# Kernel tuning notes

Hardware: AMD Instinct MI355X
Metric: run time of the kernel (lower is better)

## Reference

```python
import jax, jax.numpy as jnp
import numpy as np

CHANNELS = [64, 128, 256, 512, 512]
RES = [256, 128, 64, 32, 16]
N = 8          # batch
NQ = 128       # n_quad
NCW = 128      # nc_w (output descriptor size)
GRAD_BOOST = 10.0


def _norm(x):
    # Norm module: per-sample, per-row normalization over last dim; torch std is unbiased (ddof=1)
    m = jnp.mean(x, axis=-1, keepdims=True)
    s = jnp.std(x, axis=-1, ddof=1, keepdims=True)
    return (x - m) / (s + 1e-8)


def _quad(x, w):
    # Quad_module: (M^T @ softmax(grad_boost*w, axis=0))**2, summed over spatial dim
    n, c, h, wd = x.shape
    M = x.reshape(n, c, h * wd)                      # (N, C, HW)
    sm = jax.nn.softmax(w * GRAD_BOOST, axis=0)      # (C, NQ)
    proj = jnp.einsum('nch,co->nho', M, sm)          # (N, HW, NQ)
    return jnp.sum(proj ** 2, axis=1)                # (N, NQ)


def setup_inputs() -> dict:
    key = jax.random.key(0)
    ks = jax.random.split(key, 20)
    inp = {}
    for i, (c, r) in enumerate(zip(CHANNELS, RES)):
        inp[f"x{i}"] = jax.random.normal(ks[i], (N, c, r, r), dtype=jnp.float32)
        # torch init: 5/grad_boost * rand(n_in, n_out) = 0.5 * U[0,1)
        inp[f"w1_{i}"] = 0.5 * jax.random.uniform(ks[5 + i], (c, NQ), dtype=jnp.float32)
    d_in = len(CHANNELS) * NQ
    inp["fc1_w"] = jax.random.normal(ks[10], (d_in, 512), dtype=jnp.float32) * 0.04
    inp["fc1_b"] = jnp.zeros((512,), dtype=jnp.float32)
    inp["fc2_w"] = jax.random.normal(ks[11], (512, 512), dtype=jnp.float32) * 0.04
    inp["fc2_b"] = jnp.zeros((512,), dtype=jnp.float32)
    inp["fc3_w"] = jax.random.normal(ks[12], (512, NCW), dtype=jnp.float32) * 0.04
    inp["fc3_b"] = jnp.zeros((NCW,), dtype=jnp.float32)
    return inp


def reference(x0, x1, x2, x3, x4, w1_0, w1_1, w1_2, w1_3, w1_4,
              fc1_w, fc1_b, fc2_w, fc2_b, fc3_w, fc3_b):
    xs = [x0, x1, x2, x3, x4]
    ws = [w1_0, w1_1, w1_2, w1_3, w1_4]
    feats = [_norm(_quad(x, w)) for x, w in zip(xs, ws)]  # each (N, NQ)
    h = jnp.concatenate(feats, axis=1)                    # (N, 5*NQ)
    h = jax.nn.leaky_relu(_norm(h @ fc1_w + fc1_b), 0.01)
    h = jax.nn.leaky_relu(_norm(h @ fc2_w + fc2_b), 0.01)
    return h @ fc3_w + fc3_b                              # (N, NCW)
```

## Files before the change

### kernel.cpp

```cpp
#include <hip/hip_runtime.h>
#include <hip/hip_bf16.h>
#include <stdint.h>

#define NQ 128
#define NLVL 5

typedef float  floatx4 __attribute__((ext_vector_type(4)));
typedef short  short8  __attribute__((ext_vector_type(8)));

__device__ __forceinline__ uint16_t f2bf(float f) {
    uint32_t u = __builtin_bit_cast(uint32_t, f);
    uint32_t r = u + 0x7FFFu + ((u >> 16) & 1u);
    return (uint16_t)(r >> 16);
}
__device__ __forceinline__ uint32_t pack2(float a, float b) {
    return (uint32_t)f2bf(a) | ((uint32_t)f2bf(b) << 16);
}
__device__ __forceinline__ float bf2f(uint16_t u) {
    return __builtin_bit_cast(float, (uint32_t)u << 16);
}
__device__ __forceinline__ short8 cvt8(float4 lo, float4 hi) {
    union { short8 s; uint32_t u[4]; } r;
    r.u[0] = pack2(lo.x, lo.y);
    r.u[1] = pack2(lo.z, lo.w);
    r.u[2] = pack2(hi.x, hi.y);
    r.u[3] = pack2(hi.z, hi.w);
    return r.s;
}
__device__ __forceinline__ void split_hilo(float4 v0, float4 v1, short8& hi, short8& lo) {
    hi = cvt8(v0, v1);
    float4 r0, r1;
    r0.x = v0.x - bf2f((uint16_t)hi[0]); r0.y = v0.y - bf2f((uint16_t)hi[1]);
    r0.z = v0.z - bf2f((uint16_t)hi[2]); r0.w = v0.w - bf2f((uint16_t)hi[3]);
    r1.x = v1.x - bf2f((uint16_t)hi[4]); r1.y = v1.y - bf2f((uint16_t)hi[5]);
    r1.z = v1.z - bf2f((uint16_t)hi[6]); r1.w = v1.w - bf2f((uint16_t)hi[7]);
    lo = cvt8(r0, r1);
}

#define MFMA16(a, b, c) __builtin_amdgcn_mfma_f32_16x16x32_bf16((a), (b), (c), 0, 0, 0)


struct AParams {
    const float* x0; const float* x1;
    float*       g0; float*       g1;
    const float* w[NLVL];
    uint16_t*    smT[NLVL];
    int          C[NLVL];
};

__device__ __forceinline__ void gram_tile_diag(
    const float* __restrict__ base, int ldr, int k0, int nst,
    int m, int kg, floatx4 (&acc)[4][4])
{
    float4 Alo[4], Ahi[4], Blo[4], Bhi[4];
    {
        int k = k0 + kg * 8;
        #pragma unroll
        for (int f = 0; f < 4; ++f) {
            const float* q = base + (size_t)(f * 16 + m) * ldr + k;
            Alo[f] = *(const float4*)q; Ahi[f] = *(const float4*)(q + 4);
        }
    }
    for (int s = 0; s < nst; s += 2) {
        if (s + 1 < nst) {
            int k1 = k0 + (s + 1) * 32 + kg * 8;
            #pragma unroll
            for (int f = 0; f < 4; ++f) {
                const float* q = base + (size_t)(f * 16 + m) * ldr + k1;
                Blo[f] = *(const float4*)q; Bhi[f] = *(const float4*)(q + 4);
            }
        }
        {
            short8 fr[4];
            #pragma unroll
            for (int f = 0; f < 4; ++f) fr[f] = cvt8(Alo[f], Ahi[f]);
            #pragma unroll
            for (int rf = 0; rf < 4; ++rf)
                #pragma unroll
                for (int cf = 0; cf < 4; ++cf)
                    acc[rf][cf] = MFMA16(fr[rf], fr[cf], acc[rf][cf]);
        }
        if (s + 2 < nst) {
            int k2 = k0 + (s + 2) * 32 + kg * 8;
            #pragma unroll
            for (int f = 0; f < 4; ++f) {
                const float* q = base + (size_t)(f * 16 + m) * ldr + k2;
                Alo[f] = *(const float4*)q; Ahi[f] = *(const float4*)(q + 4);
            }
        }
        if (s + 1 < nst) {
            short8 fr[4];
            #pragma unroll
            for (int f = 0; f < 4; ++f) fr[f] = cvt8(Blo[f], Bhi[f]);
            #pragma unroll
            for (int rf = 0; rf < 4; ++rf)
                #pragma unroll
                for (int cf = 0; cf < 4; ++cf)
                    acc[rf][cf] = MFMA16(fr[rf], fr[cf], acc[rf][cf]);
        }
    }
}

__device__ __forceinline__ void gram_tile_off(
    const float* __restrict__ ab, const float* __restrict__ bb,
    int ldr, int k0, int nst, int m, int kg, floatx4 (&acc)[4][4])
{
    #pragma unroll 2
    for (int s = 0; s < nst; ++s) {
        int k = k0 + s * 32 + kg * 8;
        float4 a0[4], a1[4], b0[4], b1[4];
        #pragma unroll
        for (int f = 0; f < 4; ++f) {
            const float* qa = ab + (size_t)(f * 16 + m) * ldr + k;
            const float* qb = bb + (size_t)(f * 16 + m) * ldr + k;
            a0[f] = *(const float4*)qa; a1[f] = *(const float4*)(qa + 4);
            b0[f] = *(const float4*)qb; b1[f] = *(const float4*)(qb + 4);
        }
        short8 af[4], bf[4];
        #pragma unroll
        for (int f = 0; f < 4; ++f) {
            af[f] = cvt8(a0[f], a1[f]);
            bf[f] = cvt8(b0[f], b1[f]);
        }
        #pragma unroll
        for (int rf = 0; rf < 4; ++rf)
            #pragma unroll
            for (int cf = 0; cf < 4; ++cf)
                acc[rf][cf] = MFMA16(af[rf], bf[cf], acc[rf][cf]);
    }
}

__global__ __launch_bounds__(256) void gram_sm_kernel(AParams p) {
    __shared__ float gred[4096];
    int b  = blockIdx.x;
    int t  = threadIdx.x;
    int wv = t >> 6, lane = t & 63, m = lane & 15, kg = lane >> 4;

    if (b >= 320) {
        int idx = (b - 320) * 4 + wv;
        int lvl = idx >> 7, o = idx & 127;
        int C   = p.C[lvl];
        const float* w = p.w[lvl];
        float ev[8];
        int nIter = C >> 6;
        float mx = -1e30f;
        for (int it = 0; it < nIter; ++it) {
            float z = 10.0f * w[(size_t)(it * 64 + lane) * NQ + o];
            ev[it] = z;
            mx = fmaxf(mx, z);
        }
        #pragma unroll
        for (int s = 32; s; s >>= 1) mx = fmaxf(mx, __shfl_xor(mx, s));
        float sum = 0.f;
        for (int it = 0; it < nIter; ++it) { ev[it] = expf(ev[it] - mx); sum += ev[it]; }
        #pragma unroll
        for (int s = 32; s; s >>= 1) sum += __shfl_xor(sum, s);
        float inv = 1.0f / sum;
        uint16_t* dst = p.smT[lvl] + (size_t)o * C;
        for (int it = 0; it < nIter; ++it) dst[it * 64 + lane] = f2bf(ev[it] * inv);
        return;
    }

    floatx4 acc[4][4];
    floatx4 zero = {0.f, 0.f, 0.f, 0.f};
    #pragma unroll
    for (int i = 0; i < 4; ++i)
        #pragma unroll
        for (int j = 0; j < 4; ++j) acc[i][j] = zero;

    if (b < 256) {
        int n = b >> 5, ch = b & 31;
        const float* xb = p.x0 + (size_t)n * 64 * 65536;
        int k0 = ch * 2048 + wv * 512;
        gram_tile_diag(xb, 65536, k0, 16, m, kg, acc);

        for (int i = t; i < 4096; i += 256) gred[i] = 0.f;
        __syncthreads();
        #pragma unroll
        for (int rf = 0; rf < 4; ++rf)
            #pragma unroll
            for (int cf = 0; cf < 4; ++cf)
                #pragma unroll
                for (int r = 0; r < 4; ++r)
                    atomicAdd(&gred[(rf * 16 + kg * 4 + r) * 64 + cf * 16 + m],
                              acc[rf][cf][r]);
        __syncthreads();
        float* gb = p.g0 + (size_t)n * 4096;
        for (int i = t; i < 4096; i += 256) atomicAdd(&gb[i], gred[i]);
    } else {
        int b2 = b - 256;
        int n = b2 >> 3, kc = b2 & 7;
        const float* xb = p.x1 + (size_t)n * 128 * 16384;
        int rb = wv >> 1, cb = wv & 1;
        const float* ab = xb + (size_t)rb * 64 * 16384;
        const float* bb = xb + (size_t)cb * 64 * 16384;
        int k0 = kc * 2048;
        if (rb == cb) gram_tile_diag(ab, 16384, k0, 64, m, kg, acc);
        else          gram_tile_off(ab, bb, 16384, k0, 64, m, kg, acc);
        float* gb = p.g1 + (size_t)n * 16384;
        #pragma unroll
        for (int rf = 0; rf < 4; ++rf)
            #pragma unroll
            for (int cf = 0; cf < 4; ++cf)
                #pragma unroll
                for (int r = 0; r < 4; ++r)
                    atomicAdd(&gb[(size_t)(rb * 64 + rf * 16 + kg * 4 + r) * 128 +
                                  cb * 64 + cf * 16 + m],
                              acc[rf][cf][r]);
    }
}


struct QSParams {
    const float*    x[3];
    const uint16_t* smT[3];
    float*          quad;
    int             C[3];
    int             HW[3];
    int             blk_base[3];
    int             quad_blocks;
    const float*    g0; const float* g1;
    const uint16_t* smT0; const uint16_t* smT1;
};

template<int C>
__device__ __forceinline__ void sgs_direct(const float* __restrict__ g,
                                           const uint16_t* __restrict__ smT,
                                           float* __restrict__ qdst) {
    constexpr int RF  = C / 64;
    constexpr int KSL = C / 32;
    int t = threadIdx.x;
    int wv = t >> 6, lane = t & 63, m = lane & 15, kg = lane >> 4;
    floatx4 acc[RF][8];
    floatx4 zero = {0.f, 0.f, 0.f, 0.f};
    #pragma unroll
    for (int rf = 0; rf < RF; ++rf)
        #pragma unroll
        for (int ot = 0; ot < 8; ++ot) acc[rf][ot] = zero;

    #pragma unroll
    for (int ksl = 0; ksl < KSL; ++ksl) {
        short8 bfr[8];
        #pragma unroll
        for (int ot = 0; ot < 8; ++ot)
            bfr[ot] = *(const short8*)(smT + (size_t)(ot * 16 + m) * C + ksl * 32 + kg * 8);
        #pragma unroll
        for (int rf = 0; rf < RF; ++rf) {
            const float* gp = g + (size_t)((wv * RF + rf) * 16 + m) * C + ksl * 32 + kg * 8;
            float4 v0 = *(const float4*)gp, v1 = *(const float4*)(gp + 4);
            short8 ah, al;
            split_hilo(v0, v1, ah, al);
            #pragma unroll
            for (int ot = 0; ot < 8; ++ot) {
                acc[rf][ot] = MFMA16(ah, bfr[ot], acc[rf][ot]);
                acc[rf][ot] = MFMA16(al, bfr[ot], acc[rf][ot]);
            }
        }
    }
    #pragma unroll
    for (int ot = 0; ot < 8; ++ot) {
        float part = 0.f;
        #pragma unroll
        for (int rf = 0; rf < RF; ++rf) {
            int c0 = (wv * RF + rf) * 16 + kg * 4;
            #pragma unroll
            for (int r = 0; r < 4; ++r) {
                float sv = bf2f(smT[(size_t)(ot * 16 + m) * C + c0 + r]);
                part = fmaf(sv, acc[rf][ot][r], part);
            }
        }
        part += __shfl_xor(part, 16);
        part += __shfl_xor(part, 32);
        if (lane < 16) atomicAdd(qdst + (size_t)(ot * 16 + lane) * 16, part);
    }
}

__global__ __launch_bounds__(256) void quad_sgs_kernel(QSParams p) {
    __shared__ __align__(16) short At[64 * 40];
    __shared__ __align__(16) short Bt[128 * 40];

    int bid = blockIdx.x;
    if (bid >= p.quad_blocks) {
        int b = bid - p.quad_blocks;
        int lvl = b >> 3, n = b & 7;
        if (lvl == 0)
            sgs_direct<64>(p.g0 + (size_t)n * 4096, p.smT0,
                           p.quad + (size_t)n * 2048);
        else
            sgs_direct<128>(p.g1 + (size_t)n * 16384, p.smT1,
                            p.quad + (size_t)(8 + n) * 2048);
        return;
    }

    int lvl = 0;
    #pragma unroll
    for (int l = 1; l < 3; ++l) if (bid >= p.blk_base[l]) lvl = l;
    int rel = bid - p.blk_base[lvl];
    int n   = rel & 7;
    int ht  = rel >> 3;
    int C   = p.C[lvl];
    int HW  = p.HW[lvl];
    int h0  = ht * 64;

    const float*    xb  = p.x[lvl] + (size_t)n * C * HW + h0;
    const uint16_t* smT = p.smT[lvl];

    int t    = threadIdx.x;
    int wave = t >> 6;
    int lane = t & 63;
    int m    = lane & 15;
    int kg   = lane >> 4;

    floatx4 acc[4][2];
    floatx4 zero = {0.f, 0.f, 0.f, 0.f};
    #pragma unroll
    for (int i = 0; i < 4; ++i)
        #pragma unroll
        for (int j = 0; j < 2; ++j) acc[i][j] = zero;

    int c_l = (t & 15) * 2;
    int h_l = (t >> 4) * 4;

    for (int c0 = 0; c0 < C; c0 += 32) {
        const float* s1 = xb + (size_t)(c0 + c_l) * HW + h_l;
        float4 a4 = *(const float4*)s1;
        float4 b4 = *(const float4*)(s1 + HW);
        #pragma unroll
        for (int j = 0; j < 4; ++j) {
            uint32_t pk = (uint32_t)f2bf(((const float*)&a4)[j]) |
                          ((uint32_t)f2bf(((const float*)&b4)[j]) << 16);
            *(uint32_t*)&At[(h_l + j) * 40 + c_l] = pk;
        }
        #pragma unroll
        for (int it = 0; it < 2; ++it) {
            int idx  = it * 256 + t;
            int o    = idx >> 2;
            int part = idx & 3;
            uint4 v = *(const uint4*)(smT + (size_t)o * C + c0 + part * 8);
            *(uint4*)&Bt[o * 40 + part * 8] = v;
        }
        __syncthreads();

        short8 af[4];
        #pragma unroll
        for (int mt = 0; mt < 4; ++mt)
            af[mt] = *(const short8*)&At[(mt * 16 + m) * 40 + kg * 8];
        short8 bfr[2];
        #pragma unroll
        for (int ot = 0; ot < 2; ++ot)
            bfr[ot] = *(const short8*)&Bt[((wave * 2 + ot) * 16 + m) * 40 + kg * 8];
        #pragma unroll
        for (int mt = 0; mt < 4; ++mt)
            #pragma unroll
            for (int ot = 0; ot < 2; ++ot)
                acc[mt][ot] = MFMA16(af[mt], bfr[ot], acc[mt][ot]);
        __syncthreads();
    }

    float* qbase = p.quad + (size_t)((lvl + 2) * 8 + n) * 128 * 16;
    #pragma unroll
    for (int ot = 0; ot < 2; ++ot) {
        float part = 0.f;
        #pragma unroll
        for (int mt = 0; mt < 4; ++mt)
            #pragma unroll
            for (int r = 0; r < 4; ++r) {
                float v = acc[mt][ot][r];
                part = fmaf(v, v, part);
            }
        part += __shfl_xor(part, 16);
        part += __shfl_xor(part, 32);
        if (lane < 16) {
            int o = (wave * 2 + ot) * 16 + lane;
            atomicAdd(qbase + (size_t)o * 16, part);
        }
    }
}

__global__ __launch_bounds__(256) void hfc1_kernel(
    const float* __restrict__ quad, const float* __restrict__ w,
    const float* __restrict__ b, float* __restrict__ h1) {
    __shared__ float feat[640];
    __shared__ float stats[10];
    __shared__ float part[256];
    int blk = blockIdx.x;
    int n = blk >> 3, c8 = blk & 7;
    int t = threadIdx.x;
    for (int idx = t; idx < 640; idx += 256) {
        int L = idx >> 7, o = idx & 127;
        feat[idx] = quad[((size_t)(L * 8 + n) * 128 + o) * 16];
    }
    __syncthreads();
    int wv = t >> 6, lane = t & 63;
    for (int L = wv; L < 5; L += 4) {
        float a = feat[L * 128 + lane], c = feat[L * 128 + 64 + lane];
        float s = a + c;
        #pragma unroll
        for (int sh = 32; sh; sh >>= 1) s += __shfl_xor(s, sh);
        float mean = s * (1.f / 128.f);
        float d0 = a - mean, d1 = c - mean;
        float v = d0 * d0 + d1 * d1;
        #pragma unroll
        for (int sh = 32; sh; sh >>= 1) v += __shfl_xor(v, sh);
        if (lane == 0) {
            stats[L]     = mean;
            stats[5 + L] = 1.f / (sqrtf(v * (1.f / 127.f)) + 1e-8f);
        }
    }
    __syncthreads();
    for (int idx = t; idx < 640; idx += 256) {
        int L = idx >> 7;
        feat[idx] = (feat[idx] - stats[L]) * stats[5 + L];
    }
    __syncthreads();

    float acc = 0.f;
    const float* wc = w + c8 * 64 + lane;
    int k0 = wv * 160;
    #pragma unroll 8
    for (int k = k0; k < k0 + 160; ++k) acc = fmaf(feat[k], wc[(size_t)k * 512], acc);
    part[t] = acc;
    __syncthreads();
    if (t < 64) {
        float r = part[t] + part[t + 64] + part[t + 128] + part[t + 192];
        h1[(size_t)n * 512 + c8 * 64 + t] = r + b[c8 * 64 + t];
    }
}

__device__ __forceinline__ void norm_leaky_512(float* buf, float* red, int t) {
    float a = buf[t], c = buf[t + 256];
    float s = a + c;
    #pragma unroll
    for (int sh = 32; sh; sh >>= 1) s += __shfl_xor(s, sh);
    if ((t & 63) == 0) red[t >> 6] = s;
    __syncthreads();
    float mean = (red[0] + red[1] + red[2] + red[3]) * (1.f / 512.f);
    float d0 = a - mean, d1 = c - mean;
    float v = d0 * d0 + d1 * d1;
    #pragma unroll
    for (int sh = 32; sh; sh >>= 1) v += __shfl_xor(v, sh);
    __syncthreads();
    if ((t & 63) == 0) red[t >> 6] = v;
    __syncthreads();
    float inv = 1.f / (sqrtf((red[0] + red[1] + red[2] + red[3]) * (1.f / 511.f)) + 1e-8f);
    float n0 = d0 * inv, n1 = d1 * inv;
    buf[t]       = n0 > 0.f ? n0 : 0.01f * n0;
    buf[t + 256] = n1 > 0.f ? n1 : 0.01f * n1;
    __syncthreads();
}

__global__ __launch_bounds__(256) void hfc2_kernel(
    const float* __restrict__ h1, const float* __restrict__ w,
    const float* __restrict__ b, float* __restrict__ h2) {
    __shared__ float buf[512];
    __shared__ float red[4];
    __shared__ float part[256];
    int blk = blockIdx.x;
    int n = blk >> 3, c8 = blk & 7;
    int t = threadIdx.x;
    buf[t]       = h1[(size_t)n * 512 + t];
    buf[t + 256] = h1[(size_t)n * 512 + t + 256];
    __syncthreads();
    norm_leaky_512(buf, red, t);
    int wv = t >> 6, lane = t & 63;
    float acc = 0.f;
    const float* wc = w + c8 * 64 + lane;
    int k0 = wv * 128;
    #pragma unroll 8
    for (int k = k0; k < k0 + 128; ++k) acc = fmaf(buf[k], wc[(size_t)k * 512], acc);
    part[t] = acc;
    __syncthreads();
    if (t < 64) {
        float r = part[t] + part[t + 64] + part[t + 128] + part[t + 192];
        h2[(size_t)n * 512 + c8 * 64 + t] = r + b[c8 * 64 + t];
    }
}

__global__ __launch_bounds__(256) void hfc3_kernel(
    const float* __restrict__ h2, const float* __restrict__ w,
    const float* __restrict__ b, float* __restrict__ out) {
    __shared__ float buf[512];
    __shared__ float red[4];
    __shared__ float part[256];
    int blk = blockIdx.x;
    int n = blk >> 1, c2 = blk & 1;
    int t = threadIdx.x;
    buf[t]       = h2[(size_t)n * 512 + t];
    buf[t + 256] = h2[(size_t)n * 512 + t + 256];
    __syncthreads();
    norm_leaky_512(buf, red, t);
    int wv = t >> 6, lane = t & 63;
    float acc = 0.f;
    const float* wc = w + c2 * 64 + lane;
    int k0 = wv * 128;
    #pragma unroll 8
    for (int k = k0; k < k0 + 128; ++k) acc = fmaf(buf[k], wc[(size_t)k * 128], acc);
    part[t] = acc;
    __syncthreads();
    if (t < 64) {
        out[(size_t)n * 128 + c2 * 64 + t] =
            part[t] + part[t + 64] + part[t + 128] + part[t + 192] + b[c2 * 64 + t];
    }
}

extern "C" void kernel_launch(void* const* d_in, const int* in_sizes, int n_in,
                              void* d_out, int out_size, void* d_ws, size_t ws_size,
                              hipStream_t stream) {
    static const int Cs[NLVL]   = {64, 128, 256, 512, 512};
    static const int RESs[NLVL] = {256, 128, 64, 32, 16};

    const float* x[NLVL];
    const float* w[NLVL];
    for (int i = 0; i < NLVL; ++i) {
        x[i] = (const float*)d_in[2 * i];
        w[i] = (const float*)d_in[2 * i + 1];
    }
    const float* fc1_w = (const float*)d_in[10];
    const float* fc1_b = (const float*)d_in[11];
    const float* fc2_w = (const float*)d_in[12];
    const float* fc2_b = (const float*)d_in[13];
    const float* fc3_w = (const float*)d_in[14];
    const float* fc3_b = (const float*)d_in[15];

    uint16_t* smT_base = (uint16_t*)d_ws;
    int smOff[NLVL];
    int off = 0;
    for (int i = 0; i < NLVL; ++i) { smOff[i] = off; off += Cs[i] * NQ; }
    size_t smBytes = (size_t)off * sizeof(uint16_t);
    float* quad = (float*)((char*)d_ws + smBytes);
    size_t quadFloats = (size_t)NLVL * 8 * NQ * 16;
    float* g0 = quad + quadFloats;
    float* g1 = g0 + (size_t)8 * 64 * 64;
    float* h1 = g1 + (size_t)8 * 128 * 128;
    float* h2 = h1 + (size_t)8 * 512;
    size_t zeroBytes = (quadFloats + (size_t)8 * 64 * 64 + (size_t)8 * 128 * 128) * sizeof(float);

    hipMemsetAsync(quad, 0, zeroBytes, stream);

    AParams ap;
    ap.x0 = x[0]; ap.x1 = x[1]; ap.g0 = g0; ap.g1 = g1;
    for (int i = 0; i < NLVL; ++i) {
        ap.w[i]   = w[i];
        ap.smT[i] = smT_base + smOff[i];
        ap.C[i]   = Cs[i];
    }
    gram_sm_kernel<<<480, 256, 0, stream>>>(ap);

    QSParams qp;
    int base = 0;
    for (int i = 0; i < 3; ++i) {
        int lvl = i + 2;
        qp.x[i]   = x[lvl];
        qp.smT[i] = smT_base + smOff[lvl];
        qp.C[i]   = Cs[lvl];
        qp.HW[i]  = RESs[lvl] * RESs[lvl];
        qp.blk_base[i] = base;
        base += (RESs[lvl] * RESs[lvl] / 64) * 8;
    }
    qp.quad = quad;
    qp.quad_blocks = base;
    qp.g0 = g0; qp.g1 = g1;
    qp.smT0 = smT_base + smOff[0];
    qp.smT1 = smT_base + smOff[1];
    quad_sgs_kernel<<<base + 16, 256, 0, stream>>>(qp);

    hfc1_kernel<<<64, 256, 0, stream>>>(quad, fc1_w, fc1_b, h1);
    hfc2_kernel<<<64, 256, 0, stream>>>(h1, fc2_w, fc2_b, h2);
    hfc3_kernel<<<16, 256, 0, stream>>>(h2, fc3_w, fc3_b, (float*)d_out);
}
```

Before: 483.6 us.

## Stage Gram-matrix tiles through LDS as bf16 and widen blocks to 512 threads

The Gram kernels for levels 0 and 1 now load fp32 input chunks cooperatively, convert them to bf16 once, and stage them in padded shared memory. Waves then read MFMA fragments from there, where before each wave loaded and converted its own fragments directly from global memory. Blocks grow to 512 threads with more blocks per level, so each wave computes a smaller slice of the output tile. This removes redundant global loads and conversions, especially for level 1's off-diagonal tiles, at the cost of extra barriers per step and more atomic reductions into the global Gram buffer.

After: 423.9 us. -12.3%, faster.

```diff
diff --git a/kernel.cpp b/kernel.cpp
--- a/kernel.cpp
+++ b/kernel.cpp
@@ -48,96 +48,14 @@
     int          C[NLVL];
 };
 
-__device__ __forceinline__ void gram_tile_diag(
-    const float* __restrict__ base, int ldr, int k0, int nst,
-    int m, int kg, floatx4 (&acc)[4][4])
-{
-    float4 Alo[4], Ahi[4], Blo[4], Bhi[4];
-    {
-        int k = k0 + kg * 8;
-        #pragma unroll
-        for (int f = 0; f < 4; ++f) {
-            const float* q = base + (size_t)(f * 16 + m) * ldr + k;
-            Alo[f] = *(const float4*)q; Ahi[f] = *(const float4*)(q + 4);
-        }
-    }
-    for (int s = 0; s < nst; s += 2) {
-        if (s + 1 < nst) {
-            int k1 = k0 + (s + 1) * 32 + kg * 8;
-            #pragma unroll
-            for (int f = 0; f < 4; ++f) {
-                const float* q = base + (size_t)(f * 16 + m) * ldr + k1;
-                Blo[f] = *(const float4*)q; Bhi[f] = *(const float4*)(q + 4);
-            }
-        }
-        {
-            short8 fr[4];
-            #pragma unroll
-            for (int f = 0; f < 4; ++f) fr[f] = cvt8(Alo[f], Ahi[f]);
-            #pragma unroll
-            for (int rf = 0; rf < 4; ++rf)
-                #pragma unroll
-                for (int cf = 0; cf < 4; ++cf)
-                    acc[rf][cf] = MFMA16(fr[rf], fr[cf], acc[rf][cf]);
-        }
-        if (s + 2 < nst) {
-            int k2 = k0 + (s + 2) * 32 + kg * 8;
-            #pragma unroll
-            for (int f = 0; f < 4; ++f) {
-                const float* q = base + (size_t)(f * 16 + m) * ldr + k2;
-                Alo[f] = *(const float4*)q; Ahi[f] = *(const float4*)(q + 4);
-            }
-        }
-        if (s + 1 < nst) {
-            short8 fr[4];
-            #pragma unroll
-            for (int f = 0; f < 4; ++f) fr[f] = cvt8(Blo[f], Bhi[f]);
-            #pragma unroll
-            for (int rf = 0; rf < 4; ++rf)
-                #pragma unroll
-                for (int cf = 0; cf < 4; ++cf)
-                    acc[rf][cf] = MFMA16(fr[rf], fr[cf], acc[rf][cf]);
-        }
-    }
-}
-
-__device__ __forceinline__ void gram_tile_off(
-    const float* __restrict__ ab, const float* __restrict__ bb,
-    int ldr, int k0, int nst, int m, int kg, floatx4 (&acc)[4][4])
-{
-    #pragma unroll 2
-    for (int s = 0; s < nst; ++s) {
-        int k = k0 + s * 32 + kg * 8;
-        float4 a0[4], a1[4], b0[4], b1[4];
-        #pragma unroll
-        for (int f = 0; f < 4; ++f) {
-            const float* qa = ab + (size_t)(f * 16 + m) * ldr + k;
-            const float* qb = bb + (size_t)(f * 16 + m) * ldr + k;
-            a0[f] = *(const float4*)qa; a1[f] = *(const float4*)(qa + 4);
-            b0[f] = *(const float4*)qb; b1[f] = *(const float4*)(qb + 4);
-        }
-        short8 af[4], bf[4];
-        #pragma unroll
-        for (int f = 0; f < 4; ++f) {
-            af[f] = cvt8(a0[f], a1[f]);
-            bf[f] = cvt8(b0[f], b1[f]);
-        }
-        #pragma unroll
-        for (int rf = 0; rf < 4; ++rf)
-            #pragma unroll
-            for (int cf = 0; cf < 4; ++cf)
-                acc[rf][cf] = MFMA16(af[rf], bf[cf], acc[rf][cf]);
-    }
-}
-
-__global__ __launch_bounds__(256) void gram_sm_kernel(AParams p) {
-    __shared__ float gred[4096];
-    int b  = blockIdx.x;
-    int t  = threadIdx.x;
+__global__ __launch_bounds__(512, 5) void gram_sm_kernel(AParams p) {
+    __shared__ __align__(16) short lds[2 * 64 * 72];
+    int b = blockIdx.x;
+    int t = threadIdx.x;
     int wv = t >> 6, lane = t & 63, m = lane & 15, kg = lane >> 4;
 
-    if (b >= 320) {
-        int idx = (b - 320) * 4 + wv;
+    if (b >= 768) {
+        int idx = (b - 768) * 8 + wv;
         int lvl = idx >> 7, o = idx & 127;
         int C   = p.C[lvl];
         const float* w = p.w[lvl];
@@ -161,51 +79,128 @@
         return;
     }
 
-    floatx4 acc[4][4];
-    floatx4 zero = {0.f, 0.f, 0.f, 0.f};
-    #pragma unroll
-    for (int i = 0; i < 4; ++i)
-        #pragma unroll
-        for (int j = 0; j < 4; ++j) acc[i][j] = zero;
-
-    if (b < 256) {
-        int n = b >> 5, ch = b & 31;
+    if (b < 512) {
+        int n = b >> 6, ch = b & 63;
         const float* xb = p.x0 + (size_t)n * 64 * 65536;
-        int k0 = ch * 2048 + wv * 512;
-        gram_tile_diag(xb, 65536, k0, 16, m, kg, acc);
-
-        for (int i = t; i < 4096; i += 256) gred[i] = 0.f;
+        int rg = wv & 3, kh = wv >> 2;
+        short* buf = lds + kh * (64 * 72);
+        int tg = t & 255;
+        int k0 = ch * 1024 + kh * 512;
+
+        floatx4 acc[4];
+        floatx4 zero = {0.f, 0.f, 0.f, 0.f};
+        #pragma unroll
+        for (int cf = 0; cf < 4; ++cf) acc[cf] = zero;
+
+        float4 v[4];
+        #pragma unroll
+        for (int j = 0; j < 4; ++j) {
+            int fid = j * 256 + tg;
+            v[j] = *(const float4*)(xb + (size_t)(fid >> 4) * 65536 + k0 + (fid & 15) * 4);
+        }
+        for (int s = 0; s < 8; ++s) {
+            __syncthreads();
+            #pragma unroll
+            for (int j = 0; j < 4; ++j) {
+                int fid = j * 256 + tg;
+                uint2 pk = { pack2(v[j].x, v[j].y), pack2(v[j].z, v[j].w) };
+                *(uint2*)&buf[(fid >> 4) * 72 + (fid & 15) * 4] = pk;
+            }
+            __syncthreads();
+            if (s + 1 < 8) {
+                #pragma unroll
+                for (int j = 0; j < 4; ++j) {
+                    int fid = j * 256 + tg;
+                    v[j] = *(const float4*)(xb + (size_t)(fid >> 4) * 65536 +
+                                            k0 + (s + 1) * 64 + (fid & 15) * 4);
+                }
+            }
+            #pragma unroll
+            for (int ksl = 0; ksl < 2; ++ksl) {
+                short8 fr[4];
+                #pragma unroll
+                for (int f = 0; f < 4; ++f)
+                    fr[f] = *(const short8*)&buf[(f * 16 + m) * 72 + ksl * 32 + kg * 8];
+                short8 a = fr[rg];
+                #pragma unroll
+                for (int cf = 0; cf < 4; ++cf)
+                    acc[cf] = MFMA16(a, fr[cf], acc[cf]);
+            }
+        }
         __syncthreads();
-        #pragma unroll
-        for (int rf = 0; rf < 4; ++rf)
-            #pragma unroll
-            for (int cf = 0; cf < 4; ++cf)
-                #pragma unroll
-                for (int r = 0; r < 4; ++r)
-                    atomicAdd(&gred[(rf * 16 + kg * 4 + r) * 64 + cf * 16 + m],
-                              acc[rf][cf][r]);
+        float* gred = (float*)lds;
+        for (int i = t; i < 4096; i += 512) gred[i] = 0.f;
+        __syncthreads();
+        #pragma unroll
+        for (int cf = 0; cf < 4; ++cf)
+            #pragma unroll
+            for (int r = 0; r < 4; ++r)
+                atomicAdd(&gred[(rg * 16 + kg * 4 + r) * 64 + cf * 16 + m], acc[cf][r]);
         __syncthreads();
         float* gb = p.g0 + (size_t)n * 4096;
-        for (int i = t; i < 4096; i += 256) atomicAdd(&gb[i], gred[i]);
+        for (int i = t; i < 4096; i += 512) atomicAdd(&gb[i], gred[i]);
     } else {
-        int b2 = b - 256;
-        int n = b2 >> 3, kc = b2 & 7;
+        int b2 = b - 512;
+        int n = b2 >> 5, ch = b2 & 31;
         const float* xb = p.x1 + (size_t)n * 128 * 16384;
-        int rb = wv >> 1, cb = wv & 1;
-        const float* ab = xb + (size_t)rb * 64 * 16384;
-        const float* bb = xb + (size_t)cb * 64 * 16384;
-        int k0 = kc * 2048;
-        if (rb == cb) gram_tile_diag(ab, 16384, k0, 64, m, kg, acc);
-        else          gram_tile_off(ab, bb, 16384, k0, 64, m, kg, acc);
+        int rg = wv & 3, cg = wv >> 2;
+        int k0 = ch * 512;
+
+        floatx4 acc[2][4];
+        floatx4 zero = {0.f, 0.f, 0.f, 0.f};
+        #pragma unroll
+        for (int rf = 0; rf < 2; ++rf)
+            #pragma unroll
+            for (int cf = 0; cf < 4; ++cf) acc[rf][cf] = zero;
+
+        float4 v[4];
+        #pragma unroll
+        for (int j = 0; j < 4; ++j) {
+            int fid = j * 512 + t;
+            v[j] = *(const float4*)(xb + (size_t)(fid >> 4) * 16384 + k0 + (fid & 15) * 4);
+        }
+        for (int s = 0; s < 8; ++s) {
+            __syncthreads();
+            #pragma unroll
+            for (int j = 0; j < 4; ++j) {
+                int fid = j * 512 + t;
+                uint2 pk = { pack2(v[j].x, v[j].y), pack2(v[j].z, v[j].w) };
+                *(uint2*)&lds[(fid >> 4) * 72 + (fid & 15) * 4] = pk;
+            }
+            __syncthreads();
+            if (s + 1 < 8) {
+                #pragma unroll
+                for (int j = 0; j < 4; ++j) {
+                    int fid = j * 512 + t;
+                    v[j] = *(const float4*)(xb + (size_t)(fid >> 4) * 16384 +
+                                            k0 + (s + 1) * 64 + (fid & 15) * 4);
+                }
+            }
+            #pragma unroll
+            for (int ksl = 0; ksl < 2; ++ksl) {
+                short8 af[2], bf[4];
+                #pragma unroll
+                for (int rf = 0; rf < 2; ++rf)
+                    af[rf] = *(const short8*)&lds[(rg * 32 + rf * 16 + m) * 72 + ksl * 32 + kg * 8];
+                #pragma unroll
+                for (int cf = 0; cf < 4; ++cf)
+                    bf[cf] = *(const short8*)&lds[(cg * 64 + cf * 16 + m) * 72 + ksl * 32 + kg * 8];
+                #pragma unroll
+                for (int rf = 0; rf < 2; ++rf)
+                    #pragma unroll
+                    for (int cf = 0; cf < 4; ++cf)
+                        acc[rf][cf] = MFMA16(af[rf], bf[cf], acc[rf][cf]);
+            }
+        }
         float* gb = p.g1 + (size_t)n * 16384;
         #pragma unroll
-        for (int rf = 0; rf < 4; ++rf)
+        for (int rf = 0; rf < 2; ++rf)
             #pragma unroll
             for (int cf = 0; cf < 4; ++cf)
                 #pragma unroll
                 for (int r = 0; r < 4; ++r)
-                    atomicAdd(&gb[(size_t)(rb * 64 + rf * 16 + kg * 4 + r) * 128 +
-                                  cb * 64 + cf * 16 + m],
+                    atomicAdd(&gb[(size_t)(rg * 32 + rf * 16 + kg * 4 + r) * 128 +
+                                  cg * 64 + cf * 16 + m],
                               acc[rf][cf][r]);
     }
 }
@@ -544,7 +539,7 @@
         ap.smT[i] = smT_base + smOff[i];
         ap.C[i]   = Cs[i];
     }
-    gram_sm_kernel<<<480, 256, 0, stream>>>(ap);
+    gram_sm_kernel<<<848, 512, 0, stream>>>(ap);
 
     QSParams qp;
     int base = 0;
```
